# Performance work log

Measured on AMD Instinct MI355X. Metric: run time of the kernel, lower is better.

The kernel has to match this reference:

```python
import jax, jax.numpy as jnp
import numpy as np

N_TARGETS = 4
BATCH_SIZE = 4
B = N_TARGETS * BATCH_SIZE
N_SAMPLES = 1024
LAYERS = [(128, 128), (256, 64), (512, 32)]  # (channels, spatial)
EPS_COS = 1e-10


def setup_inputs() -> dict:
    key = jax.random.key(0)
    inp = {}
    for l, (c, s) in enumerate(LAYERS):
        k1, k2, k3, k4, key = jax.random.split(key, 5)
        n = s * s
        inp[f't{l}'] = jax.random.normal(k1, (N_TARGETS, c, s, s), dtype=jnp.float32)
        inp[f'g{l}'] = jax.random.normal(k2, (B, c, s, s), dtype=jnp.float32)
        inp[f'ix{l}'] = jax.random.randint(k3, (B, N_SAMPLES), 0, n)
        inp[f'iy{l}'] = jax.random.randint(k4, (B, N_SAMPLES), 0, n)
    return inp


def _cos_remd(x, y):
    # x: (b,n,c), y: (b,m,c)
    xn = jnp.linalg.norm(x, axis=2, keepdims=True)            # (b,n,1)
    yn = jnp.linalg.norm(y, axis=2, keepdims=True)            # (b,m,1)
    cross = jnp.einsum('bnc,bmc->bnm', x, y)                  # (b,n,m)
    dist = 1.0 - cross / (xn * yn.transpose(0, 2, 1) + EPS_COS)
    m1 = dist.min(axis=1).mean(axis=1)                        # min over n, mean over m
    m2 = dist.min(axis=2).mean(axis=1)                        # min over m, mean over n
    return jnp.maximum(m1, m2)                                # (b,)


def _moment_loss(x, y):
    mu_x = x.mean(axis=1, keepdims=True)
    mu_y = y.mean(axis=1, keepdims=True)
    mu_diff = jnp.abs(mu_x - mu_y).mean(axis=(1, 2))
    x_c = x - mu_x
    y_c = y - mu_y
    x_cov = jnp.einsum('bnc,bnd->bcd', x_c, x_c) / (x.shape[1] - 1)
    y_cov = jnp.einsum('bmc,bmd->bcd', y_c, y_c) / (y.shape[1] - 1)
    cov_diff = jnp.abs(x_cov - y_cov).mean(axis=(1, 2))
    return mu_diff + cov_diff                                 # (b,)


def _layer_loss(t, g, ix, iy):
    b, c, h, w = g.shape
    y = jnp.tile(t, (BATCH_SIZE, 1, 1, 1)).reshape(b, t.shape[1], -1)  # (b,c,n_y)
    x = g.reshape(b, c, -1)                                            # (b,c,n_x)
    x = jnp.take_along_axis(x, ix[:, None, :], axis=2)                 # (b,c,ns)
    y = jnp.take_along_axis(y, iy[:, None, :], axis=2)                 # (b,c,ns)
    x = x.transpose(0, 2, 1)
    y = y.transpose(0, 2, 1)
    return _cos_remd(x, y) + _moment_loss(x, y)


def reference(t0, g0, t1, g1, t2, g2, ix0, iy0, ix1, iy1, ix2, iy2):
    loss = (_layer_loss(t0, g0, ix0, iy0)
            + _layer_loss(t1, g1, ix1, iy1)
            + _layer_loss(t2, g2, ix2, iy2))
    return loss.reshape(BATCH_SIZE, N_TARGETS).mean(axis=0)   # (n_targets,)
```

## Files before the change

kernel.cpp:

```cpp
#include <hip/hip_runtime.h>
#include <math.h>

#define NT 4
#define BSZ 4
#define BB 16
#define NS 1024
#define MAXL 3

typedef unsigned short u16;
typedef __attribute__((ext_vector_type(8))) short bf16x8;
typedef __attribute__((ext_vector_type(4))) float f32x4;

struct LayerP {
    const float *g, *t;
    const int *ix, *iy;
    u16 *Xt, *Yt, *Xs, *Ys;
    float *xp, *yp;
    float *xcs, *ycs;
    float *rxn, *ryn;
    float *sx, *sy;
    unsigned *m1u, *m2u;
    float *cov;
    int C, n, nchunk, ntri, lid, xblk, yblk;
};
struct Tab {
    LayerP L[MAXL];
    int nl, nb, b0;
    float* losspart;
};

__device__ __forceinline__ unsigned fenc(float f) {
    unsigned u = __float_as_uint(f);
    return (u & 0x80000000u) ? ~u : (u | 0x80000000u);
}
__device__ __forceinline__ float fdec(unsigned u) {
    unsigned v = (u & 0x80000000u) ? (u & 0x7FFFFFFFu) : ~u;
    return __uint_as_float(v);
}
__device__ __forceinline__ u16 f2bf(float f) {
    unsigned u = __float_as_uint(f);
    unsigned r = u + 0x7FFFu + ((u >> 16) & 1u);
    return (u16)(r >> 16);
}
__device__ __forceinline__ float bf2f(u16 h) {
    return __uint_as_float((unsigned)h << 16);
}

__global__ __launch_bounds__(256) void gather(Tab tab)
{
    int f = blockIdx.x;
    int l = 0, side = 0;
    #pragma unroll
    for (int li = 0; li < MAXL; ++li) {
        if (li >= tab.nl) break;
        if (f < tab.L[li].xblk) { l = li; side = 0; goto decoded; }
        f -= tab.L[li].xblk;
        if (f < tab.L[li].yblk) { l = li; side = 1; goto decoded; }
        f -= tab.L[li].yblk;
    }
decoded:;
    const LayerP P = tab.L[l];
    int ng = P.C >> 6;
    int cgi = f % ng; f /= ng;
    int sq = f & 3; f >>= 2;
    int bl = f;
    int bg = tab.b0 + bl;
    int c0 = cgi * 64;
    int tid = threadIdx.x;
    int s = sq * 256 + tid;
    int n = P.n;
    int idx = side ? P.iy[bg * NS + s] : P.ix[bg * NS + s];
    const float* __restrict__ src =
        (side ? P.t + ((size_t)(bg % NT) * P.C + c0) * n
              : P.g + ((size_t)bg * P.C + c0) * n) + idx;
    u16* __restrict__ dst = (side ? P.Yt : P.Xt) + ((size_t)bl * P.C + c0) * NS + s;
    float v[64];
    #pragma unroll
    for (int j = 0; j < 64; ++j) v[j] = src[(size_t)j * n];
    #pragma unroll
    for (int j = 0; j < 64; ++j) dst[(size_t)j * NS] = f2bf(v[j]);
}

__global__ void transpose_k(Tab tab)
{
    int x = blockIdx.x, l = 0;
    while (l < MAXL - 1 && x >= tab.L[l].C / 64) { x -= tab.L[l].C / 64; ++l; }
    const LayerP P = tab.L[l];
    int z = blockIdx.z;
    int bl = z >> 1, which = z & 1;
    const u16* __restrict__ Zt = which ? P.Yt : P.Xt;
    u16* __restrict__ Zs = which ? P.Ys : P.Xs;
    float* __restrict__ zp = which ? P.yp : P.xp;
    float* __restrict__ zcs = which ? P.ycs : P.xcs;
    int C = P.C;
    int ctile = x;
    int c0 = ctile * 64, s0 = blockIdx.y * 64;
    int stile = blockIdx.y;
    __shared__ __align__(16) u16 T[64][72];
    int tid = threadIdx.x;
    #pragma unroll
    for (int rep = 0; rep < 2; ++rep) {
        int q = tid + rep * 256;
        int rr = q >> 3, seg = q & 7;
        float4 f4 = *(const float4*)&Zt[((size_t)bl * C + c0 + rr) * NS + s0 + seg * 8];
        *(float4*)&T[rr][seg * 8] = f4;
        const u16* hp = (const u16*)&f4;
        float p = 0.f;
        #pragma unroll
        for (int e = 0; e < 8; ++e) p += bf2f(hp[e]);
        p += __shfl_xor(p, 1);
        p += __shfl_xor(p, 2);
        p += __shfl_xor(p, 4);
        if (seg == 0)
            zcs[(((size_t)bl * P.nchunk + ctile) * 16 + stile) * 64 + rr] = p;
    }
    __syncthreads();
    #pragma unroll
    for (int rep = 0; rep < 2; ++rep) {
        int q = tid + rep * 256;
        int sr = q >> 3, cs = q & 7;
        __align__(16) u16 tmp[8];
        float p = 0.f;
        #pragma unroll
        for (int e = 0; e < 8; ++e) {
            u16 h = T[cs * 8 + e][sr];
            tmp[e] = h;
            float v = bf2f(h);
            p = fmaf(v, v, p);
        }
        *(float4*)&Zs[((size_t)bl * NS + s0 + sr) * C + c0 + cs * 8] = *(float4*)tmp;
        p += __shfl_xor(p, 1);
        p += __shfl_xor(p, 2);
        p += __shfl_xor(p, 4);
        if (cs == 0)
            zp[((size_t)bl * P.nchunk + ctile) * NS + s0 + sr] = p;
    }
}

__global__ void colnorm_reduce(Tab tab)
{
    const LayerP P = tab.L[blockIdx.y];
    int bl = blockIdx.z;
    int s = blockIdx.x * 256 + threadIdx.x;
    float ax = 0.f, ay = 0.f;
    for (int k = 0; k < P.nchunk; ++k) {
        size_t o = ((size_t)bl * P.nchunk + k) * NS + s;
        ax += P.xp[o];
        ay += P.yp[o];
    }
    P.rxn[bl * NS + s] = rsqrtf(ax);
    P.ryn[bl * NS + s] = rsqrtf(ay);
    P.m1u[bl * NS + s] = 0xFFFFFFFFu;
    P.m2u[bl * NS + s] = 0xFFFFFFFFu;
    int cq = P.C >> 2;
    for (int c = blockIdx.x * cq + threadIdx.x; c < (blockIdx.x + 1) * cq; c += 256) {
        int ct = c >> 6, cr = c & 63;
        float sx = 0.f, sy = 0.f;
        for (int st = 0; st < 16; ++st) {
            size_t o = (((size_t)bl * P.nchunk + ct) * 16 + st) * 64 + cr;
            sx += P.xcs[o];
            sy += P.ycs[o];
        }
        P.sx[bl * P.C + c] = sx;
        P.sy[bl * P.C + c] = sy;
    }
}

__global__ __launch_bounds__(256) void cross_mfma(Tab tab)
{
    int z = blockIdx.z;
    int l = z / tab.nb, bl = z - l * tab.nb;
    const LayerP P = tab.L[l];
    int C = P.C;
    int i0 = blockIdx.x * 128, j0 = blockIdx.y * 128;
    __shared__ __align__(16) u16 As[128][40], Bs[128][40];
    int tid = threadIdx.x;
    int w = tid >> 6, lane = tid & 63;
    int wr = w >> 1, wc = w & 1;
    int q = lane >> 4, r = lane & 15;
    const u16* __restrict__ Xb = P.Xs + ((size_t)bl * NS + i0) * C;
    const u16* __restrict__ Yb = P.Ys + ((size_t)bl * NS + j0) * C;
    f32x4 acc[4][4];
    #pragma unroll
    for (int m = 0; m < 4; ++m)
        #pragma unroll
        for (int nn = 0; nn < 4; ++nn) acc[m][nn] = (f32x4){0.f, 0.f, 0.f, 0.f};

    for (int kk = 0; kk < C; kk += 32) {
        __syncthreads();
        #pragma unroll
        for (int rep = 0; rep < 2; ++rep) {
            int qid = tid + rep * 256;
            int row = qid >> 2, seg = qid & 3;
            size_t off = (size_t)row * C + kk + seg * 8;
            *(float4*)&As[row][seg * 8] = *(const float4*)&Xb[off];
            *(float4*)&Bs[row][seg * 8] = *(const float4*)&Yb[off];
        }
        __syncthreads();
        bf16x8 a[4], b[4];
        #pragma unroll
        for (int m = 0; m < 4; ++m)
            a[m] = *(const bf16x8*)&As[wr * 64 + m * 16 + r][q * 8];
        #pragma unroll
        for (int nn = 0; nn < 4; ++nn)
            b[nn] = *(const bf16x8*)&Bs[wc * 64 + nn * 16 + r][q * 8];
        #pragma unroll
        for (int m = 0; m < 4; ++m)
            #pragma unroll
            for (int nn = 0; nn < 4; ++nn)
                acc[m][nn] = __builtin_amdgcn_mfma_f32_16x16x32_bf16(a[m], b[nn], acc[m][nn], 0, 0, 0);
    }

    float rxl[4][4], ryl[4];
    #pragma unroll
    for (int m = 0; m < 4; ++m)
        #pragma unroll
        for (int reg = 0; reg < 4; ++reg)
            rxl[m][reg] = P.rxn[bl * NS + i0 + wr * 64 + m * 16 + q * 4 + reg];
    #pragma unroll
    for (int nn = 0; nn < 4; ++nn)
        ryl[nn] = P.ryn[bl * NS + j0 + wc * 64 + nn * 16 + r];

    float rm[4][4], cm[4];
    #pragma unroll
    for (int m = 0; m < 4; ++m)
        #pragma unroll
        for (int reg = 0; reg < 4; ++reg) rm[m][reg] = 1e30f;
    #pragma unroll
    for (int nn = 0; nn < 4; ++nn) cm[nn] = 1e30f;
    #pragma unroll
    for (int m = 0; m < 4; ++m)
        #pragma unroll
        for (int nn = 0; nn < 4; ++nn)
            #pragma unroll
            for (int reg = 0; reg < 4; ++reg) {
                float d = 1.f - acc[m][nn][reg] * rxl[m][reg] * ryl[nn];
                rm[m][reg] = fminf(rm[m][reg], d);
                cm[nn] = fminf(cm[nn], d);
            }
    #pragma unroll
    for (int m = 0; m < 4; ++m)
        #pragma unroll
        for (int reg = 0; reg < 4; ++reg) {
            float v = rm[m][reg];
            v = fminf(v, __shfl_xor(v, 1));
            v = fminf(v, __shfl_xor(v, 2));
            v = fminf(v, __shfl_xor(v, 4));
            v = fminf(v, __shfl_xor(v, 8));
            rm[m][reg] = v;
        }
    if (r == 0) {
        #pragma unroll
        for (int m = 0; m < 4; ++m)
            #pragma unroll
            for (int reg = 0; reg < 4; ++reg) {
                int i = i0 + wr * 64 + m * 16 + q * 4 + reg;
                atomicMin(&P.m2u[bl * NS + i], fenc(rm[m][reg]));
            }
    }
    #pragma unroll
    for (int nn = 0; nn < 4; ++nn) {
        float v = cm[nn];
        v = fminf(v, __shfl_xor(v, 16));
        v = fminf(v, __shfl_xor(v, 32));
        cm[nn] = v;
    }
    if (q == 0) {
        #pragma unroll
        for (int nn = 0; nn < 4; ++nn) {
            int j = j0 + wc * 64 + nn * 16 + r;
            atomicMin(&P.m1u[bl * NS + j], fenc(cm[nn]));
        }
    }
}

__global__ __launch_bounds__(256) void cov_mfma(Tab tab)
{
    int x = blockIdx.x, l = 0;
    while (l < MAXL - 1 && x >= tab.L[l].ntri) { x -= tab.L[l].ntri; ++l; }
    const LayerP P = tab.L[l];
    int u = x;
    int bl = blockIdx.y;
    int C = P.C;
    int ty = 0;
    while ((ty + 1) * (ty + 2) / 2 <= u) ++ty;
    int tx = u - ty * (ty + 1) / 2;
    int c0 = ty * 128, d0 = tx * 128;
    float wgt = (tx == ty) ? 1.f : 2.f;

    __shared__ __align__(16) u16 As[128][40], Bs[128][40], Cs2[128][40], Ds[128][40];
    int tid = threadIdx.x;
    int w = tid >> 6, lane = tid & 63;
    int wr = w >> 1, wc = w & 1;
    int q = lane >> 4, r = lane & 15;
    const u16* __restrict__ Xc = P.Xt + ((size_t)bl * C + c0) * NS;
    const u16* __restrict__ Xd = P.Xt + ((size_t)bl * C + d0) * NS;
    const u16* __restrict__ Yc = P.Yt + ((size_t)bl * C + c0) * NS;
    const u16* __restrict__ Yd = P.Yt + ((size_t)bl * C + d0) * NS;

    f32x4 accX[4][4], accY[4][4];
    #pragma unroll
    for (int m = 0; m < 4; ++m)
        #pragma unroll
        for (int nn = 0; nn < 4; ++nn) {
            accX[m][nn] = (f32x4){0.f, 0.f, 0.f, 0.f};
            accY[m][nn] = (f32x4){0.f, 0.f, 0.f, 0.f};
        }

    for (int ss = 0; ss < NS; ss += 32) {
        __syncthreads();
        #pragma unroll
        for (int rep = 0; rep < 2; ++rep) {
            int qid = tid + rep * 256;
            int row = qid >> 2, seg = qid & 3;
            size_t off = (size_t)row * NS + ss + seg * 8;
            *(float4*)&As[row][seg * 8]  = *(const float4*)&Xc[off];
            *(float4*)&Bs[row][seg * 8]  = *(const float4*)&Xd[off];
            *(float4*)&Cs2[row][seg * 8] = *(const float4*)&Yc[off];
            *(float4*)&Ds[row][seg * 8]  = *(const float4*)&Yd[off];
        }
        __syncthreads();
        {
            bf16x8 a[4], b[4];
            #pragma unroll
            for (int m = 0; m < 4; ++m) a[m] = *(const bf16x8*)&As[wr * 64 + m * 16 + r][q * 8];
            #pragma unroll
            for (int nn = 0; nn < 4; ++nn) b[nn] = *(const bf16x8*)&Bs[wc * 64 + nn * 16 + r][q * 8];
            #pragma unroll
            for (int m = 0; m < 4; ++m)
                #pragma unroll
                for (int nn = 0; nn < 4; ++nn)
                    accX[m][nn] = __builtin_amdgcn_mfma_f32_16x16x32_bf16(a[m], b[nn], accX[m][nn], 0, 0, 0);
        }
        {
            bf16x8 a[4], b[4];
            #pragma unroll
            for (int m = 0; m < 4; ++m) a[m] = *(const bf16x8*)&Cs2[wr * 64 + m * 16 + r][q * 8];
            #pragma unroll
            for (int nn = 0; nn < 4; ++nn) b[nn] = *(const bf16x8*)&Ds[wc * 64 + nn * 16 + r][q * 8];
            #pragma unroll
            for (int m = 0; m < 4; ++m)
                #pragma unroll
                for (int nn = 0; nn < 4; ++nn)
                    accY[m][nn] = __builtin_amdgcn_mfma_f32_16x16x32_bf16(a[m], b[nn], accY[m][nn], 0, 0, 0);
        }
    }

    float scxv[4][4], scyv[4][4], sdxv[4], sdyv[4];
    #pragma unroll
    for (int m = 0; m < 4; ++m)
        #pragma unroll
        for (int reg = 0; reg < 4; ++reg) {
            int c = c0 + wr * 64 + m * 16 + q * 4 + reg;
            scxv[m][reg] = P.sx[bl * C + c];
            scyv[m][reg] = P.sy[bl * C + c];
        }
    #pragma unroll
    for (int nn = 0; nn < 4; ++nn) {
        int d = d0 + wc * 64 + nn * 16 + r;
        sdxv[nn] = P.sx[bl * C + d];
        sdyv[nn] = P.sy[bl * C + d];
    }
    const float invNS = 1.f / NS, invNSm1 = 1.f / (NS - 1);
    float tsum = 0.f;
    #pragma unroll
    for (int m = 0; m < 4; ++m)
        #pragma unroll
        for (int nn = 0; nn < 4; ++nn)
            #pragma unroll
            for (int reg = 0; reg < 4; ++reg) {
                float cx = (accX[m][nn][reg] - scxv[m][reg] * sdxv[nn] * invNS) * invNSm1;
                float cy = (accY[m][nn][reg] - scyv[m][reg] * sdyv[nn] * invNS) * invNSm1;
                tsum += fabsf(cx - cy);
            }
    tsum *= wgt;
    __shared__ float redc[4];
    for (int o = 32; o > 0; o >>= 1) tsum += __shfl_down(tsum, o);
    if (lane == 0) redc[w] = tsum;
    __syncthreads();
    if (tid == 0)
        P.cov[(size_t)bl * P.ntri + u] = redc[0] + redc[1] + redc[2] + redc[3];
}

__global__ void finalize_kernel(Tab tab)
{
    const LayerP P = tab.L[blockIdx.x];
    int bl = blockIdx.y;
    int tid = threadIdx.x;
    int C = P.C;
    float s1 = 0.f, s2 = 0.f, smu = 0.f, scov = 0.f;
    for (int s = tid; s < NS; s += 256) {
        s1 += fdec(P.m1u[bl * NS + s]);
        s2 += fdec(P.m2u[bl * NS + s]);
    }
    for (int c = tid; c < C; c += 256) smu += fabsf(P.sx[bl * C + c] - P.sy[bl * C + c]);
    for (int i = tid; i < P.ntri; i += 256) scov += P.cov[(size_t)bl * P.ntri + i];
    __shared__ float red[4][4];
    for (int o = 32; o > 0; o >>= 1) {
        s1 += __shfl_down(s1, o);
        s2 += __shfl_down(s2, o);
        smu += __shfl_down(smu, o);
        scov += __shfl_down(scov, o);
    }
    int wid = tid >> 6, lane = tid & 63;
    if (lane == 0) { red[0][wid] = s1; red[1][wid] = s2; red[2][wid] = smu; red[3][wid] = scov; }
    __syncthreads();
    if (tid == 0) {
        s1 = red[0][0] + red[0][1] + red[0][2] + red[0][3];
        s2 = red[1][0] + red[1][1] + red[1][2] + red[1][3];
        smu = red[2][0] + red[2][1] + red[2][2] + red[2][3];
        scov = red[3][0] + red[3][1] + red[3][2] + red[3][3];
        float m1m = s1 * (1.f / NS), m2m = s2 * (1.f / NS);
        float mu_diff = smu * (1.f / NS) * (1.f / (float)C);
        float cov_diff = scov / ((float)C * (float)C);
        tab.losspart[(tab.b0 + bl) * 3 + P.lid] = fmaxf(m1m, m2m) + mu_diff + cov_diff;
    }
}

__global__ void out_kernel(const float* __restrict__ lp, float* __restrict__ out)
{
    int t = threadIdx.x;
    if (t < NT) {
        float s = 0.f;
        for (int k = 0; k < BSZ; ++k)
            for (int l = 0; l < 3; ++l)
                s += lp[(k * NT + t) * 3 + l];
        out[t] = s * (1.f / BSZ);
    }
}

static inline size_t alignup(size_t v) { return (v + 255) & ~(size_t)255; }

static size_t layer_bytes(int C, int n, int nb) {
    int nchunk = C / 64;
    int tc = C / 128, ntri = tc * (tc + 1) / 2;
    size_t szZ = alignup((size_t)NS * C * 2);
    size_t szP = alignup((size_t)nchunk * NS * 4);
    size_t szCS = alignup((size_t)nb * nchunk * 16 * 64 * 4);
    return (size_t)nb * (4 * szZ + 2 * szP + 4 * alignup(NS * 4)
                         + 2 * alignup(C * 4) + alignup(ntri * 4))
           + 2 * szCS;
}

static char* fill_layer(LayerP& P, char* p, int C, int n, int nb, int lid,
                        const float* g, const float* t, const int* ix, const int* iy) {
    P.g = g; P.t = t; P.ix = ix; P.iy = iy;
    P.C = C; P.n = n; P.lid = lid;
    P.nchunk = C / 64;
    int tc = C / 128;
    P.ntri = tc * (tc + 1) / 2;
    P.xblk = (C / 64) * 4 * nb;
    P.yblk = (C / 64) * 4 * nb;
    size_t szZ = alignup((size_t)NS * C * 2);
    size_t szP = alignup((size_t)P.nchunk * NS * 4);
    size_t szCS = alignup((size_t)nb * P.nchunk * 16 * 64 * 4);
    P.Xt = (u16*)p;  p += nb * szZ;
    P.Yt = (u16*)p;  p += nb * szZ;
    P.Xs = (u16*)p;  p += nb * szZ;
    P.Ys = (u16*)p;  p += nb * szZ;
    P.xp = (float*)p; p += nb * szP;
    P.yp = (float*)p; p += nb * szP;
    P.xcs = (float*)p; p += szCS;
    P.ycs = (float*)p; p += szCS;
    P.rxn = (float*)p; p += nb * alignup(NS * 4);
    P.ryn = (float*)p; p += nb * alignup(NS * 4);
    P.m1u = (unsigned*)p; p += nb * alignup(NS * 4);
    P.m2u = (unsigned*)p; p += nb * alignup(NS * 4);
    P.sx = (float*)p; p += nb * alignup(C * 4);
    P.sy = (float*)p; p += nb * alignup(C * 4);
    P.cov = (float*)p; p += nb * alignup(P.ntri * 4);
    return p;
}

static void launch_group(const Tab& tab, hipStream_t stream) {
    int sumC64 = 0, sumNtri = 0, flatN = 0;
    for (int l = 0; l < tab.nl; ++l) {
        sumC64 += tab.L[l].C / 64;
        sumNtri += tab.L[l].ntri;
        flatN += tab.L[l].xblk + tab.L[l].yblk;
    }
    int nb = tab.nb;
    gather<<<flatN, 256, 0, stream>>>(tab);
    transpose_k<<<dim3(sumC64, NS / 64, nb * 2), 256, 0, stream>>>(tab);
    colnorm_reduce<<<dim3(NS / 256, tab.nl, nb), 256, 0, stream>>>(tab);
    cross_mfma<<<dim3(NS / 128, NS / 128, tab.nl * nb), 256, 0, stream>>>(tab);
    cov_mfma<<<dim3(sumNtri, nb), 256, 0, stream>>>(tab);
    finalize_kernel<<<dim3(tab.nl, nb), 256, 0, stream>>>(tab);
}

extern "C" void kernel_launch(void* const* d_in, const int* in_sizes, int n_in,
                              void* d_out, int out_size, void* d_ws, size_t ws_size,
                              hipStream_t stream)
{
    const float* tp[3] = {(const float*)d_in[0], (const float*)d_in[4], (const float*)d_in[8]};
    const float* gp[3] = {(const float*)d_in[1], (const float*)d_in[5], (const float*)d_in[9]};
    const int* ixp[3]  = {(const int*)d_in[2], (const int*)d_in[6], (const int*)d_in[10]};
    const int* iyp[3]  = {(const int*)d_in[3], (const int*)d_in[7], (const int*)d_in[11]};
    const int Cs[3] = {128, 256, 512};
    const int Sp[3] = {128, 64, 32};

    float* out = (float*)d_out;
    char* ws = (char*)d_ws;
    float* losspart = (float*)ws;
    size_t base = alignup(BB * 3 * 4);
    size_t avail = (ws_size > base) ? ws_size - base : 0;

    size_t need_all = 0;
    for (int l = 0; l < 3; ++l) need_all += layer_bytes(Cs[l], Sp[l] * Sp[l], BB);

    if (avail >= need_all) {
        Tab tab;
        tab.nl = 3; tab.nb = BB; tab.b0 = 0; tab.losspart = losspart;
        char* p = ws + base;
        for (int l = 0; l < 3; ++l)
            p = fill_layer(tab.L[l], p, Cs[l], Sp[l] * Sp[l], BB, l,
                           gp[l], tp[l], ixp[l], iyp[l]);
        launch_group(tab, stream);
    } else {
        for (int l = 0; l < 3; ++l) {
            size_t per_b = layer_bytes(Cs[l], Sp[l] * Sp[l], 1);
            int G = (int)(avail / per_b);
            if (G > BB) G = BB;
            if (G < 1) G = 1;
            for (int b0 = 0; b0 < BB; b0 += G) {
                int nb = (BB - b0 < G) ? (BB - b0) : G;
                Tab tab;
                tab.nl = 1; tab.nb = nb; tab.b0 = b0; tab.losspart = losspart;
                fill_layer(tab.L[0], ws + base, Cs[l], Sp[l] * Sp[l], nb, l,
                           gp[l], tp[l], ixp[l], iyp[l]);
                launch_group(tab, stream);
            }
        }
    }
    out_kernel<<<1, 64, 0, stream>>>(losspart, out);
}
```

Before: 276.6 us.

## Stream whole rows into LDS for gather and use direct global-to-LDS tile loads

The gather kernel now gives one 64-thread block per (channel, batch, slice). It streams the entire source row into shared memory with double-buffered global_load_lds and then picks out the sampled indices locally, replacing scattered strided global reads. Per-channel sums move from the transpose kernel into the gather kernel, and the reduce step is adjusted to match. The MFMA cross and covariance kernels load their tiles with global_load_lds into unpadded LDS arrays. The row streaming reads full rows instead of 1024 samples, and removing the padding may add LDS bank conflicts.

```diff
diff --git a/kernel.cpp b/kernel.cpp
--- a/kernel.cpp
+++ b/kernel.cpp
@@ -16,12 +16,12 @@
     const int *ix, *iy;
     u16 *Xt, *Yt, *Xs, *Ys;
     float *xp, *yp;
-    float *xcs, *ycs;
+    float *psx, *psy;
     float *rxn, *ryn;
     float *sx, *sy;
     unsigned *m1u, *m2u;
     float *cov;
-    int C, n, nchunk, ntri, lid, xblk, yblk;
+    int C, n, nchunk, ntri, lid, hs, xblk, yblk;
 };
 struct Tab {
     LayerP L[MAXL];
@@ -46,7 +46,13 @@
     return __uint_as_float((unsigned)h << 16);
 }
 
-__global__ __launch_bounds__(256) void gather(Tab tab)
+__device__ __forceinline__ void gload16(const void* src, void* dst) {
+    __builtin_amdgcn_global_load_lds(
+        (const __attribute__((address_space(1))) float*)src,
+        (__attribute__((address_space(3))) float*)dst, 16, 0, 0);
+}
+
+__global__ __launch_bounds__(64) void gather(Tab tab)
 {
     int f = blockIdx.x;
     int l = 0, side = 0;
@@ -60,25 +66,62 @@
     }
 decoded:;
     const LayerP P = tab.L[l];
-    int ng = P.C >> 6;
-    int cgi = f % ng; f /= ng;
-    int sq = f & 3; f >>= 2;
-    int bl = f;
+    int c = f % P.C; f /= P.C;
+    int bl = f % tab.nb;
+    int h = f / tab.nb;
     int bg = tab.b0 + bl;
-    int c0 = cgi * 64;
-    int tid = threadIdx.x;
-    int s = sq * 256 + tid;
-    int n = P.n;
-    int idx = side ? P.iy[bg * NS + s] : P.ix[bg * NS + s];
-    const float* __restrict__ src =
-        (side ? P.t + ((size_t)(bg % NT) * P.C + c0) * n
-              : P.g + ((size_t)bg * P.C + c0) * n) + idx;
-    u16* __restrict__ dst = (side ? P.Yt : P.Xt) + ((size_t)bl * P.C + c0) * NS + s;
-    float v[64];
-    #pragma unroll
-    for (int j = 0; j < 64; ++j) v[j] = src[(size_t)j * n];
-    #pragma unroll
-    for (int j = 0; j < 64; ++j) dst[(size_t)j * NS] = f2bf(v[j]);
+    int lane = threadIdx.x;
+
+    int slice = P.n / P.hs;
+    int chf = slice < 1024 ? slice : 1024;
+    int nch = slice / chf;
+    int sbase = h * slice;
+    __shared__ __align__(16) float buf[2][1024];
+
+    const float* __restrict__ row = side
+        ? P.t + ((size_t)(bg % NT) * P.C + c) * P.n
+        : P.g + ((size_t)bg * P.C + c) * P.n;
+    const int* __restrict__ idx = (side ? P.iy : P.ix) + bg * NS;
+
+    int px[16];
+    float xv[16];
+    #pragma unroll
+    for (int j = 0; j < 16; ++j) { px[j] = idx[lane + j * 64] - sbase; xv[j] = 0.f; }
+
+    int ipc = chf >> 8;
+    int npro = nch < 2 ? nch : 2;
+    for (int d = 0; d < npro; ++d)
+        for (int i = 0; i < ipc; ++i)
+            gload16(row + sbase + d * chf + i * 256 + lane * 4, &buf[d][i * 256]);
+
+    for (int k = 0; k < nch; ++k) {
+        if (k + 1 < nch) asm volatile("s_waitcnt vmcnt(4)" ::: "memory");
+        else             asm volatile("s_waitcnt vmcnt(0)" ::: "memory");
+        __builtin_amdgcn_sched_barrier(0);
+        int lo = k * chf;
+        #pragma unroll
+        for (int j = 0; j < 16; ++j) {
+            int rel = px[j] - lo;
+            if ((unsigned)rel < (unsigned)chf) xv[j] = buf[k & 1][rel];
+        }
+        if (k + 2 < nch)
+            for (int i = 0; i < ipc; ++i)
+                gload16(row + sbase + (k + 2) * chf + i * 256 + lane * 4, &buf[k & 1][i * 256]);
+    }
+
+    u16* __restrict__ out = (side ? P.Yt : P.Xt) + ((size_t)bl * P.C + c) * NS;
+    float ax = 0.f;
+    #pragma unroll
+    for (int j = 0; j < 16; ++j) {
+        if ((unsigned)px[j] < (unsigned)slice) {
+            u16 hb = f2bf(xv[j]);
+            out[lane + j * 64] = hb;
+            ax += bf2f(hb);
+        }
+    }
+    for (int o = 32; o > 0; o >>= 1) ax += __shfl_down(ax, o);
+    if (lane == 0)
+        (side ? P.psy : P.psx)[((size_t)h * tab.nb + bl) * P.C + c] = ax;
 }
 
 __global__ void transpose_k(Tab tab)
@@ -91,28 +134,17 @@
     const u16* __restrict__ Zt = which ? P.Yt : P.Xt;
     u16* __restrict__ Zs = which ? P.Ys : P.Xs;
     float* __restrict__ zp = which ? P.yp : P.xp;
-    float* __restrict__ zcs = which ? P.ycs : P.xcs;
     int C = P.C;
     int ctile = x;
     int c0 = ctile * 64, s0 = blockIdx.y * 64;
-    int stile = blockIdx.y;
     __shared__ __align__(16) u16 T[64][72];
     int tid = threadIdx.x;
     #pragma unroll
     for (int rep = 0; rep < 2; ++rep) {
         int q = tid + rep * 256;
         int rr = q >> 3, seg = q & 7;
-        float4 f4 = *(const float4*)&Zt[((size_t)bl * C + c0 + rr) * NS + s0 + seg * 8];
-        *(float4*)&T[rr][seg * 8] = f4;
-        const u16* hp = (const u16*)&f4;
-        float p = 0.f;
-        #pragma unroll
-        for (int e = 0; e < 8; ++e) p += bf2f(hp[e]);
-        p += __shfl_xor(p, 1);
-        p += __shfl_xor(p, 2);
-        p += __shfl_xor(p, 4);
-        if (seg == 0)
-            zcs[(((size_t)bl * P.nchunk + ctile) * 16 + stile) * 64 + rr] = p;
+        *(float4*)&T[rr][seg * 8] =
+            *(const float4*)&Zt[((size_t)bl * C + c0 + rr) * NS + s0 + seg * 8];
     }
     __syncthreads();
     #pragma unroll
@@ -141,6 +173,7 @@
 {
     const LayerP P = tab.L[blockIdx.y];
     int bl = blockIdx.z;
+    int nb = tab.nb;
     int s = blockIdx.x * 256 + threadIdx.x;
     float ax = 0.f, ay = 0.f;
     for (int k = 0; k < P.nchunk; ++k) {
@@ -154,12 +187,10 @@
     P.m2u[bl * NS + s] = 0xFFFFFFFFu;
     int cq = P.C >> 2;
     for (int c = blockIdx.x * cq + threadIdx.x; c < (blockIdx.x + 1) * cq; c += 256) {
-        int ct = c >> 6, cr = c & 63;
         float sx = 0.f, sy = 0.f;
-        for (int st = 0; st < 16; ++st) {
-            size_t o = (((size_t)bl * P.nchunk + ct) * 16 + st) * 64 + cr;
-            sx += P.xcs[o];
-            sy += P.ycs[o];
+        for (int h = 0; h < P.hs; ++h) {
+            sx += P.psx[((size_t)h * nb + bl) * P.C + c];
+            sy += P.psy[((size_t)h * nb + bl) * P.C + c];
         }
         P.sx[bl * P.C + c] = sx;
         P.sy[bl * P.C + c] = sy;
@@ -173,11 +204,12 @@
     const LayerP P = tab.L[l];
     int C = P.C;
     int i0 = blockIdx.x * 128, j0 = blockIdx.y * 128;
-    __shared__ __align__(16) u16 As[128][40], Bs[128][40];
+    __shared__ __align__(16) u16 As[128][32], Bs[128][32];
     int tid = threadIdx.x;
     int w = tid >> 6, lane = tid & 63;
     int wr = w >> 1, wc = w & 1;
     int q = lane >> 4, r = lane & 15;
+    int lrow = lane >> 2, lseg = (lane & 3) * 8;
     const u16* __restrict__ Xb = P.Xs + ((size_t)bl * NS + i0) * C;
     const u16* __restrict__ Yb = P.Ys + ((size_t)bl * NS + j0) * C;
     f32x4 acc[4][4];
@@ -189,12 +221,10 @@
     for (int kk = 0; kk < C; kk += 32) {
         __syncthreads();
         #pragma unroll
-        for (int rep = 0; rep < 2; ++rep) {
-            int qid = tid + rep * 256;
-            int row = qid >> 2, seg = qid & 3;
-            size_t off = (size_t)row * C + kk + seg * 8;
-            *(float4*)&As[row][seg * 8] = *(const float4*)&Xb[off];
-            *(float4*)&Bs[row][seg * 8] = *(const float4*)&Yb[off];
+        for (int it = 0; it < 2; ++it) {
+            int br = (it * 4 + w) * 16;
+            gload16(Xb + (size_t)(br + lrow) * C + kk + lseg, &As[br][0]);
+            gload16(Yb + (size_t)(br + lrow) * C + kk + lseg, &Bs[br][0]);
         }
         __syncthreads();
         bf16x8 a[4], b[4];
@@ -288,11 +318,12 @@
     int c0 = ty * 128, d0 = tx * 128;
     float wgt = (tx == ty) ? 1.f : 2.f;
 
-    __shared__ __align__(16) u16 As[128][40], Bs[128][40], Cs2[128][40], Ds[128][40];
+    __shared__ __align__(16) u16 As[128][32], Bs[128][32], Cs2[128][32], Ds[128][32];
     int tid = threadIdx.x;
     int w = tid >> 6, lane = tid & 63;
     int wr = w >> 1, wc = w & 1;
     int q = lane >> 4, r = lane & 15;
+    int lrow = lane >> 2, lseg = (lane & 3) * 8;
     const u16* __restrict__ Xc = P.Xt + ((size_t)bl * C + c0) * NS;
     const u16* __restrict__ Xd = P.Xt + ((size_t)bl * C + d0) * NS;
     const u16* __restrict__ Yc = P.Yt + ((size_t)bl * C + c0) * NS;
@@ -310,14 +341,13 @@
     for (int ss = 0; ss < NS; ss += 32) {
         __syncthreads();
         #pragma unroll
-        for (int rep = 0; rep < 2; ++rep) {
-            int qid = tid + rep * 256;
-            int row = qid >> 2, seg = qid & 3;
-            size_t off = (size_t)row * NS + ss + seg * 8;
-            *(float4*)&As[row][seg * 8]  = *(const float4*)&Xc[off];
-            *(float4*)&Bs[row][seg * 8]  = *(const float4*)&Xd[off];
-            *(float4*)&Cs2[row][seg * 8] = *(const float4*)&Yc[off];
-            *(float4*)&Ds[row][seg * 8]  = *(const float4*)&Yd[off];
+        for (int it = 0; it < 2; ++it) {
+            int br = (it * 4 + w) * 16;
+            size_t roff = (size_t)(br + lrow) * NS + ss + lseg;
+            gload16(Xc + roff, &As[br][0]);
+            gload16(Xd + roff, &Bs[br][0]);
+            gload16(Yc + roff, &Cs2[br][0]);
+            gload16(Yd + roff, &Ds[br][0]);
         }
         __syncthreads();
         {
@@ -431,15 +461,18 @@
 
 static inline size_t alignup(size_t v) { return (v + 255) & ~(size_t)255; }
 
+static int slices_of(int n) { int hs = n / 4096; return hs < 1 ? 1 : hs; }
+
 static size_t layer_bytes(int C, int n, int nb) {
     int nchunk = C / 64;
     int tc = C / 128, ntri = tc * (tc + 1) / 2;
+    int hs = slices_of(n);
     size_t szZ = alignup((size_t)NS * C * 2);
     size_t szP = alignup((size_t)nchunk * NS * 4);
-    size_t szCS = alignup((size_t)nb * nchunk * 16 * 64 * 4);
+    size_t szPS = alignup((size_t)hs * nb * C * 4);
     return (size_t)nb * (4 * szZ + 2 * szP + 4 * alignup(NS * 4)
                          + 2 * alignup(C * 4) + alignup(ntri * 4))
-           + 2 * szCS;
+           + 2 * szPS;
 }
 
 static char* fill_layer(LayerP& P, char* p, int C, int n, int nb, int lid,
@@ -449,19 +482,20 @@
     P.nchunk = C / 64;
     int tc = C / 128;
     P.ntri = tc * (tc + 1) / 2;
-    P.xblk = (C / 64) * 4 * nb;
-    P.yblk = (C / 64) * 4 * nb;
+    P.hs = slices_of(n);
+    P.xblk = C * P.hs * nb;
+    P.yblk = C * P.hs * nb;
     size_t szZ = alignup((size_t)NS * C * 2);
     size_t szP = alignup((size_t)P.nchunk * NS * 4);
-    size_t szCS = alignup((size_t)nb * P.nchunk * 16 * 64 * 4);
+    size_t szPS = alignup((size_t)P.hs * nb * C * 4);
     P.Xt = (u16*)p;  p += nb * szZ;
     P.Yt = (u16*)p;  p += nb * szZ;
     P.Xs = (u16*)p;  p += nb * szZ;
     P.Ys = (u16*)p;  p += nb * szZ;
     P.xp = (float*)p; p += nb * szP;
     P.yp = (float*)p; p += nb * szP;
-    P.xcs = (float*)p; p += szCS;
-    P.ycs = (float*)p; p += szCS;
+    P.psx = (float*)p; p += szPS;
+    P.psy = (float*)p; p += szPS;
     P.rxn = (float*)p; p += nb * alignup(NS * 4);
     P.ryn = (float*)p; p += nb * alignup(NS * 4);
     P.m1u = (unsigned*)p; p += nb * alignup(NS * 4);
@@ -480,7 +514,7 @@
         flatN += tab.L[l].xblk + tab.L[l].yblk;
     }
     int nb = tab.nb;
-    gather<<<flatN, 256, 0, stream>>>(tab);
+    gather<<<flatN, 64, 0, stream>>>(tab);
     transpose_k<<<dim3(sumC64, NS / 64, nb * 2), 256, 0, stream>>>(tab);
     colnorm_reduce<<<dim3(NS / 256, tab.nl, nb), 256, 0, stream>>>(tab);
     cross_mfma<<<dim3(NS / 128, NS / 128, tab.nl * nb), 256, 0, stream>>>(tab);
```

After: 228.1 us. 17.5% less time.
